# Optimization experiments

Hardware: AMD Instinct MI355X
Metric: run time of the kernel (lower is better)

The kernel has to match this reference:

```python
import jax, jax.numpy as jnp
import numpy as np

EPS_LN = 1e-6
EPS_NORM = 1e-12
MAX_SCALE_MUL = float(np.log(100.0))
H = 16  # num_heads


def _ln(x):
    # affine-free LayerNorm over last dim (torch uses biased variance)
    mu = jnp.mean(x, axis=-1, keepdims=True)
    var = jnp.mean((x - mu) ** 2, axis=-1, keepdims=True)
    return (x - mu) / jnp.sqrt(var + EPS_LN)


def _l2norm(x):
    n = jnp.sqrt(jnp.sum(x * x, axis=-1, keepdims=True))
    return x / jnp.maximum(n, EPS_NORM)


def setup_inputs() -> dict:
    key = jax.random.key(0)
    ks = jax.random.split(key, 12)
    B, L, C = 4, 1024, 1024
    Ccond, Dff = 1024, 4096
    s = lambda fan: 1.0 / np.sqrt(fan)
    return {
        "x": jax.random.normal(ks[0], (B, L, C), jnp.float32),
        "cond": jax.random.normal(ks[1], (B, Ccond), jnp.float32),
        "mat_qkv_w": jax.random.normal(ks[2], (3 * C, C), jnp.float32) * s(C),
        "q_bias": jnp.zeros((C,), jnp.float32),
        "v_bias": jnp.zeros((C,), jnp.float32),
        "scale_mul": jnp.full((1, H, 1, 1), np.log(4.0), jnp.float32),
        "proj_w": jax.random.normal(ks[3], (C, C), jnp.float32) * s(C),
        "proj_b": jnp.zeros((C,), jnp.float32),
        "ada_w": jax.random.normal(ks[4], (6 * C, Ccond), jnp.float32) * s(Ccond),
        "ada_b": jnp.zeros((6 * C,), jnp.float32),
        "fc1_w": jax.random.normal(ks[5], (Dff, C), jnp.float32) * s(C),
        "fc1_b": jnp.zeros((Dff,), jnp.float32),
        "fc2_w": jax.random.normal(ks[6], (C, Dff), jnp.float32) * s(Dff),
        "fc2_b": jnp.zeros((C,), jnp.float32),
    }


def reference(x, cond, mat_qkv_w, q_bias, v_bias, scale_mul, proj_w, proj_b,
              ada_w, ada_b, fc1_w, fc1_b, fc2_w, fc2_b):
    B, L, C = x.shape
    hd = C // H

    # AdaLN modulation params: SiLU -> Linear -> [B,1,6,C]
    ada = jax.nn.silu(cond) @ ada_w.T + ada_b
    ada = ada.reshape(B, 1, 6, C)
    gamma1, gamma2, scale1, scale2, shift1, shift2 = [ada[:, :, i] for i in range(6)]

    # --- attention branch ---
    x1 = _ln(x) * (scale1 + 1.0) + shift1
    qkv_bias = jnp.concatenate([q_bias, jnp.zeros_like(q_bias), v_bias])
    qkv = (x1 @ mat_qkv_w.T + qkv_bias).reshape(B, L, 3, H, hd)
    q, k, v = [jnp.transpose(qkv[:, :, i], (0, 2, 1, 3)) for i in range(3)]  # [B,H,L,hd]

    sm = jnp.exp(jnp.minimum(scale_mul, MAX_SCALE_MUL))  # [1,H,1,1]
    q = _l2norm(q) * sm
    k = _l2norm(k)

    scores = jnp.einsum('bhqd,bhkd->bhqk', q, k)  # scale = 1.0 under l2 norm
    probs = jax.nn.softmax(scores, axis=-1)
    o = jnp.einsum('bhqk,bhkd->bhqd', probs, v)
    o = jnp.transpose(o, (0, 2, 1, 3)).reshape(B, L, C)
    attn_out = o @ proj_w.T + proj_b
    x = x + attn_out * gamma1

    # --- FFN branch ---
    x2 = _ln(x) * (scale2 + 1.0) + shift2
    h = jax.nn.gelu(x2 @ fc1_w.T + fc1_b, approximate=False)
    ffn_out = h @ fc2_w.T + fc2_b
    x = x + ffn_out * gamma2
    return x
```

## Files before the change

### kernel.cpp

```cpp
#include <hip/hip_runtime.h>

typedef __bf16 bf16x8_t __attribute__((ext_vector_type(8)));
typedef bf16x8_t bf16x8 __attribute__((may_alias));
typedef float f32x4 __attribute__((ext_vector_type(4)));
typedef unsigned short u16x4 __attribute__((ext_vector_type(4)));
typedef unsigned short u16x8 __attribute__((ext_vector_type(8)));

#define DEV __device__ __forceinline__

DEV float b2f(unsigned short u) {
  union { unsigned int i; float f; } x; x.i = ((unsigned int)u) << 16; return x.f;
}
DEV unsigned short f2b(float f) {
  union { float f; unsigned int i; } x; x.f = f;
  return (unsigned short)((x.i + 0x7fffu + ((x.i >> 16) & 1u)) >> 16);
}

#define AS1(p) ((__attribute__((address_space(1))) void*)(p))
#define AS3(p) ((__attribute__((address_space(3))) void*)(p))

__global__ __launch_bounds__(256) void k_ada(const float* __restrict__ cond,
                                             const float* __restrict__ w,
                                             const float* __restrict__ bias,
                                             float* __restrict__ out) {
  __shared__ float sc[4096];
  int tt = threadIdx.x;
#pragma unroll
  for (int i = 0; i < 16; ++i) {
    float v = cond[tt + i * 256];
    sc[tt + i * 256] = v / (1.f + __expf(-v));
  }
  __syncthreads();
  int j = blockIdx.x * 4 + (tt >> 6);
  int lane = tt & 63;
  const float* wr = w + (size_t)j * 1024;
  float s0 = 0.f, s1 = 0.f, s2 = 0.f, s3 = 0.f;
#pragma unroll
  for (int u = 0; u < 4; ++u) {
    int k = u * 256 + lane * 4;
    float4 a = *(const float4*)(wr + k);
    float4 c0 = *(const float4*)(sc + k);
    float4 c1 = *(const float4*)(sc + 1024 + k);
    float4 c2 = *(const float4*)(sc + 2048 + k);
    float4 c3 = *(const float4*)(sc + 3072 + k);
    s0 += a.x * c0.x + a.y * c0.y + a.z * c0.z + a.w * c0.w;
    s1 += a.x * c1.x + a.y * c1.y + a.z * c1.z + a.w * c1.w;
    s2 += a.x * c2.x + a.y * c2.y + a.z * c2.z + a.w * c2.w;
    s3 += a.x * c3.x + a.y * c3.y + a.z * c3.z + a.w * c3.w;
  }
#pragma unroll
  for (int o = 1; o < 64; o <<= 1) {
    s0 += __shfl_xor(s0, o); s1 += __shfl_xor(s1, o);
    s2 += __shfl_xor(s2, o); s3 += __shfl_xor(s3, o);
  }
  if (lane == 0) {
    float bb = bias[j];
    out[j] = s0 + bb;
    out[6144 + j] = s1 + bb;
    out[12288 + j] = s2 + bb;
    out[18432 + j] = s3 + bb;
  }
}

__global__ __launch_bounds__(256) void k_castall(const float* __restrict__ q,
                                                 const float* __restrict__ p,
                                                 const float* __restrict__ f1,
                                                 const float* __restrict__ f2,
                                                 unsigned short* __restrict__ wq,
                                                 unsigned short* __restrict__ wp,
                                                 unsigned short* __restrict__ wf1,
                                                 unsigned short* __restrict__ wf2) {
  int i = blockIdx.x * 256 + threadIdx.x;
  for (int v = i; v < 3145728; v += 524288) {
    const float* s; unsigned short* d; int off;
    if (v < 786432) { s = q; d = wq; off = v; }
    else if (v < 1048576) { s = p; d = wp; off = v - 786432; }
    else if (v < 2097152) { s = f1; d = wf1; off = v - 1048576; }
    else { s = f2; d = wf2; off = v - 2097152; }
    float4 x = ((const float4*)s)[off];
    u16x4 o;
    o[0] = f2b(x.x); o[1] = f2b(x.y); o[2] = f2b(x.z); o[3] = f2b(x.w);
    *(u16x4*)(d + (size_t)off * 4) = o;
  }
}

__global__ __launch_bounds__(256) void k_ln_mod(const float* __restrict__ src,
                                                const float* __restrict__ ada,
                                                unsigned short* __restrict__ dst,
                                                int sidx, int hidx) {
  int row = blockIdx.x;
  int b = row >> 10;
  int t = threadIdx.x, lane = t & 63, wv = t >> 6;
  float4 v = *(const float4*)(src + (size_t)row * 1024 + t * 4);
  float s = v.x + v.y + v.z + v.w;
  float s2 = v.x * v.x + v.y * v.y + v.z * v.z + v.w * v.w;
#pragma unroll
  for (int o = 1; o < 64; o <<= 1) { s += __shfl_xor(s, o); s2 += __shfl_xor(s2, o); }
  __shared__ float red[8];
  if (lane == 0) { red[wv] = s; red[4 + wv] = s2; }
  __syncthreads();
  float ts = red[0] + red[1] + red[2] + red[3];
  float ts2 = red[4] + red[5] + red[6] + red[7];
  float mu = ts * (1.f / 1024.f);
  float var = ts2 * (1.f / 1024.f) - mu * mu;
  float rstd = rsqrtf(var + 1e-6f);
  const float* ar = ada + (size_t)b * 6144;
  float4 sc = *(const float4*)(ar + sidx * 1024 + t * 4);
  float4 sh = *(const float4*)(ar + hidx * 1024 + t * 4);
  u16x4 o;
  o[0] = f2b((v.x - mu) * rstd * (sc.x + 1.f) + sh.x);
  o[1] = f2b((v.y - mu) * rstd * (sc.y + 1.f) + sh.y);
  o[2] = f2b((v.z - mu) * rstd * (sc.z + 1.f) + sh.z);
  o[3] = f2b((v.w - mu) * rstd * (sc.w + 1.f) + sh.w);
  *(u16x4*)(dst + (size_t)row * 1024 + t * 4) = o;
}

template <int EPI, int SPLIT>
__global__ __launch_bounds__(512, 4) void k_gemm256(const unsigned short* __restrict__ A,
                                                    const unsigned short* __restrict__ W,
                                                    int N, int lda, int ldb, int nt,
                                                    const float* __restrict__ bias,
                                                    const float* __restrict__ qb,
                                                    const float* __restrict__ vb,
                                                    unsigned short* __restrict__ o0,
                                                    unsigned short* __restrict__ o1,
                                                    unsigned short* __restrict__ o2,
                                                    unsigned short* __restrict__ o3) {
  __shared__ unsigned short LDS[36864];
  const int tid = threadIdx.x;
  const int wv = tid >> 6, lane = tid & 63;
  const int fr = lane & 15, fg = lane >> 4;
  const int wm = wv >> 1, wn = wv & 1;

  const int cpx = gridDim.x >> 3;
  int wid = ((int)blockIdx.x & 7) * cpx + ((int)blockIdx.x >> 3);
  int sp = 0;
  if (SPLIT > 1) { sp = wid & (SPLIT - 1); wid >>= 2; }
  const int nx = N >> 7;
  const int m0 = (wid / nx) * 256, n0 = (wid % nx) * 128;
  const int kbase = sp * (nt << 5);
  unsigned short* outp = (SPLIT > 1) ? (sp == 0 ? o0 : sp == 1 ? o1 : sp == 2 ? o2 : o3) : o0;

  const int sRow = tid >> 2;
  const int sCh = (tid & 3) ^ ((tid >> 3) & 3);
  const unsigned short* aG = A + (size_t)(m0 + sRow) * lda + kbase + sCh * 8;
  const unsigned short* bG = W + (size_t)(n0 + sRow) * ldb + kbase + sCh * 8;

#define STQ3(qi_)                                                                            \
  {                                                                                          \
    unsigned short* d_ = LDS + ((qi_) % 3) * 12288 + tid * 8;                                \
    const int ko_ = (qi_) * 32;                                                              \
    __builtin_amdgcn_global_load_lds(AS1(aG + ko_), AS3(d_), 16, 0, 0);                      \
    __builtin_amdgcn_global_load_lds(AS1(aG + (size_t)128 * lda + ko_), AS3(d_ + 4096), 16, 0, 0); \
    __builtin_amdgcn_global_load_lds(AS1(bG + ko_), AS3(d_ + 8192), 16, 0, 0);               \
  }

  const int rswz = (fr >> 1) & 3;
  const int xc = (fg ^ rswz) << 3;
  const int aOff = (wm * 64 + fr) * 32 + xc;
  const int bOff = 8192 + (wn * 64 + fr) * 32 + xc;

  f32x4 zz = {0.f, 0.f, 0.f, 0.f};
  f32x4 acc[4][4];
#pragma unroll
  for (int i = 0; i < 4; ++i)
#pragma unroll
    for (int j = 0; j < 4; ++j) acc[i][j] = zz;

  STQ3(0); STQ3(1); STQ3(2);
  asm volatile("s_waitcnt vmcnt(6)" ::: "memory");
  __builtin_amdgcn_s_barrier();

#define LDSV(off) (*(const bf16x8*)(LDS + (off)))

  for (int t = 0; t < nt; ++t) {
    if (t >= 1 && t + 2 < nt) STQ3(t + 2);
    const int REG = (t % 3) * 12288;
    bf16x8 b0 = LDSV(REG + bOff);
    bf16x8 b1 = LDSV(REG + bOff + 512);
    bf16x8 b2 = LDSV(REG + bOff + 1024);
    bf16x8 b3 = LDSV(REG + bOff + 1536);
    __builtin_amdgcn_s_setprio(1);
#pragma unroll
    for (int mi = 0; mi < 4; ++mi) {
      bf16x8 a = LDSV(REG + aOff + mi * 512);
      acc[mi][0] = __builtin_amdgcn_mfma_f32_16x16x32_bf16(a, b0, acc[mi][0], 0, 0, 0);
      acc[mi][1] = __builtin_amdgcn_mfma_f32_16x16x32_bf16(a, b1, acc[mi][1], 0, 0, 0);
      acc[mi][2] = __builtin_amdgcn_mfma_f32_16x16x32_bf16(a, b2, acc[mi][2], 0, 0, 0);
      acc[mi][3] = __builtin_amdgcn_mfma_f32_16x16x32_bf16(a, b3, acc[mi][3], 0, 0, 0);
    }
    __builtin_amdgcn_s_setprio(0);
    if (t < nt - 1) {
      if (t + 2 < nt) {
        asm volatile("s_waitcnt vmcnt(3)" ::: "memory");
      } else {
        asm volatile("s_waitcnt vmcnt(0)" ::: "memory");
      }
      __builtin_amdgcn_s_barrier();
    }
  }

  if constexpr (EPI == 0) {
    const int nb = n0 + wn * 64;
    if (nb < 2048) {
      const bool isq = nb < 1024;
      const int h = (nb & 1023) >> 6;
      const float sm = isq ? __expf(fminf(bias[h], 4.6051701859880914f)) : 1.f;
      unsigned short* obase = isq ? o0 : o1;
#pragma unroll
      for (int mi = 0; mi < 4; ++mi) {
#pragma unroll
        for (int r = 0; r < 4; ++r) {
          float v0 = acc[mi][0][r], v1 = acc[mi][1][r], v2 = acc[mi][2][r], v3 = acc[mi][3][r];
          if (isq) {
            v0 += qb[nb + fr]; v1 += qb[nb + 16 + fr];
            v2 += qb[nb + 32 + fr]; v3 += qb[nb + 48 + fr];
          }
          float ss = v0 * v0 + v1 * v1 + v2 * v2 + v3 * v3;
          ss += __shfl_xor(ss, 1); ss += __shfl_xor(ss, 2);
          ss += __shfl_xor(ss, 4); ss += __shfl_xor(ss, 8);
          float scl = sm / fmaxf(sqrtf(ss), 1e-12f);
          int m = m0 + wm * 64 + mi * 16 + fg * 4 + r;
          int b = m >> 10, l = m & 1023;
          unsigned short* dst = obase + ((size_t)(b * 16 + h) * 1024 + l) * 64 + fr;
          dst[0]  = f2b(v0 * scl);
          dst[16] = f2b(v1 * scl);
          dst[32] = f2b(v2 * scl);
          dst[48] = f2b(v3 * scl);
        }
      }
    } else {
#pragma unroll
      for (int mi = 0; mi < 4; ++mi)
#pragma unroll
        for (int ni = 0; ni < 4; ++ni)
#pragma unroll
          for (int r = 0; r < 4; ++r) {
            int m = m0 + wm * 64 + mi * 16 + fg * 4 + r;
            int n = nb + ni * 16 + fr - 2048;
            o2[(size_t)m * 1024 + n] = f2b(acc[mi][ni][r] + vb[n]);
          }
    }
  } else {
#pragma unroll
    for (int mi = 0; mi < 4; ++mi) {
#pragma unroll
      for (int ni = 0; ni < 4; ++ni) {
#pragma unroll
        for (int r = 0; r < 4; ++r) {
          int m = m0 + wm * 64 + mi * 16 + fg * 4 + r;
          int n = n0 + wn * 64 + ni * 16 + fr;
          float v = acc[mi][ni][r];
          if constexpr (EPI == 2) {
            float z = v + bias[n];
            float u = z * (0.7978845608f + 0.0356774081f * z * z);
            float e = __expf(2.f * u);
            float th = 1.f - 2.f / (e + 1.f);
            outp[(size_t)m * N + n] = f2b(0.5f * z * (1.f + th));
          } else {
            outp[(size_t)m * N + n] = f2b(v);
          }
        }
      }
    }
  }
#undef STQ3
#undef LDSV
}

__global__ __launch_bounds__(256) void k_fc2red(const unsigned short* __restrict__ P0,
                                                const unsigned short* __restrict__ P1,
                                                const unsigned short* __restrict__ P2,
                                                const unsigned short* __restrict__ P3,
                                                const float* __restrict__ xmid,
                                                const float* __restrict__ bias,
                                                const float* __restrict__ ada,
                                                float* __restrict__ out) {
  size_t idx = ((size_t)blockIdx.x * 256 + threadIdx.x) * 8;
  int n = (int)(idx & 1023);
  int b = (int)(idx >> 20);
  u16x8 v0 = *(const u16x8*)(P0 + idx);
  u16x8 v1 = *(const u16x8*)(P1 + idx);
  u16x8 v2 = *(const u16x8*)(P2 + idx);
  u16x8 v3 = *(const u16x8*)(P3 + idx);
  const float* gp = ada + (size_t)b * 6144 + 1024 + n;
  const float* bp = bias + n;
  const float* xp = xmid + idx;
  float* op = out + idx;
#pragma unroll
  for (int i = 0; i < 8; ++i) {
    float sum = b2f(v0[i]) + b2f(v1[i]) + b2f(v2[i]) + b2f(v3[i]);
    op[i] = xp[i] + (sum + bp[i]) * gp[i];
  }
}

__global__ __launch_bounds__(512) void k_gemm8(const unsigned short* __restrict__ A,
                                               const unsigned short* __restrict__ W,
                                               int M, int N, int K, int Khalf,
                                               const float* __restrict__ bias,
                                               const float* __restrict__ resid,
                                               const float* __restrict__ ada,
                                               float* __restrict__ outp) {
  __shared__ unsigned short SM[49152];
  const int t = threadIdx.x, lane = t & 63, wv = t >> 6;
  const int grp = wv >> 2, w4 = wv & 3;
  const int wr = w4 >> 1, wc = w4 & 1;
  const int cpx = gridDim.x >> 3;
  const int orig = blockIdx.x;
  const int wid = (orig & 7) * cpx + (orig >> 3);
  const int nx = N >> 7;
  const int m0 = (wid / nx) * 128, n0 = (wid % nx) * 128;

  f32x4 zz = {0.f, 0.f, 0.f, 0.f};
  f32x4 acc[4][4];
#pragma unroll
  for (int i = 0; i < 4; ++i)
#pragma unroll
    for (int j = 0; j < 4; ++j) acc[i][j] = zz;

  const int srow = lane >> 2, scol = (lane & 3) * 8;
  const int kbase = grp * Khalf;
  const unsigned short* aSrc0 = A + (size_t)(m0 + w4 * 16 + srow) * K + kbase + scol;
  const unsigned short* aSrc1 = aSrc0 + (size_t)64 * K;
  const unsigned short* bSrc0 = W + (size_t)(n0 + w4 * 16 + srow) * K + kbase + scol;
  const unsigned short* bSrc1 = bSrc0 + (size_t)64 * K;
  unsigned short* grpA = SM + grp * 24576;

  const int fr = lane & 15, fk = (lane >> 4) * 8;

#define STG8(buf_, k0_)                                                                            \
  {                                                                                                \
    __builtin_amdgcn_global_load_lds(AS1(aSrc0 + (k0_)), AS3(grpA + (buf_)*8192 + w4 * 512), 16, 0, 0); \
    __builtin_amdgcn_global_load_lds(AS1(aSrc1 + (k0_)), AS3(grpA + (buf_)*8192 + 2048 + w4 * 512), 16, 0, 0); \
    __builtin_amdgcn_global_load_lds(AS1(bSrc0 + (k0_)), AS3(grpA + (buf_)*8192 + 4096 + w4 * 512), 16, 0, 0); \
    __builtin_amdgcn_global_load_lds(AS1(bSrc1 + (k0_)), AS3(grpA + (buf_)*8192 + 6144 + w4 * 512), 16, 0, 0); \
  }

  const int nsteps = Khalf >> 5;
  STG8(0, 0);
  STG8(1, 32);
  asm volatile("s_waitcnt vmcnt(4)" ::: "memory");
  __builtin_amdgcn_s_barrier();

  for (int i = 0; i < nsteps; ++i) {
    const int buf = i % 3;
    if (i + 2 < nsteps) STG8((i + 2) % 3, (i + 2) * 32);
    const unsigned short* aRd = grpA + buf * 8192 + (wr * 64 + fr) * 32 + fk;
    const unsigned short* bRd = grpA + buf * 8192 + 4096 + (wc * 64 + fr) * 32 + fk;
    bf16x8 af[4], bfv[4];
#pragma unroll
    for (int q = 0; q < 4; ++q) af[q] = *(const bf16x8*)(aRd + q * 512);
#pragma unroll
    for (int q = 0; q < 4; ++q) bfv[q] = *(const bf16x8*)(bRd + q * 512);
    __builtin_amdgcn_s_setprio(1);
#pragma unroll
    for (int mi = 0; mi < 4; ++mi)
#pragma unroll
      for (int ni = 0; ni < 4; ++ni)
        acc[mi][ni] = __builtin_amdgcn_mfma_f32_16x16x32_bf16(af[mi], bfv[ni], acc[mi][ni], 0, 0, 0);
    __builtin_amdgcn_s_setprio(0);
    if (i < nsteps - 1) {
      if (i + 2 < nsteps) {
        asm volatile("s_waitcnt vmcnt(4)" ::: "memory");
      } else {
        asm volatile("s_waitcnt vmcnt(0)" ::: "memory");
      }
      __builtin_amdgcn_s_barrier();
    }
  }
  __syncthreads();

  float* xch = (float*)SM;
#pragma unroll
  for (int c = 0; c < 16; ++c) {
    if (grp == 1)
      *(f32x4*)&xch[c * 1024 + (w4 * 64 + lane) * 4] = acc[c >> 2][c & 3];
  }
  __syncthreads();
  if (grp == 1) return;
#pragma unroll
  for (int c = 0; c < 16; ++c) {
    f32x4 p = *(const f32x4*)&xch[c * 1024 + (w4 * 64 + lane) * 4];
    acc[c >> 2][c & 3] += p;
  }

  const int fg = lane >> 4;
#pragma unroll
  for (int mi = 0; mi < 4; ++mi) {
#pragma unroll
    for (int ni = 0; ni < 4; ++ni) {
#pragma unroll
      for (int r = 0; r < 4; ++r) {
        int m = m0 + wr * 64 + mi * 16 + fg * 4 + r;
        int n = n0 + wc * 64 + ni * 16 + fr;
        float v = acc[mi][ni][r];
        float g = ada[(size_t)(m >> 10) * 6144 + n];
        outp[(size_t)m * N + n] = resid[(size_t)m * N + n] + (v + bias[n]) * g;
      }
    }
  }
#undef STG8
}

__global__ __launch_bounds__(256) void k_vtrans(const unsigned short* __restrict__ V,
                                                unsigned short* __restrict__ Vt) {
  int bh = blockIdx.y, b = bh >> 4, h = bh & 15;
  int l0 = blockIdx.x * 64;
  __shared__ unsigned short tile[64][72];
  int t = threadIdx.x;
  int lr = t >> 2, dp = (t & 3) * 16;
  const unsigned short* src = V + (size_t)(b * 1024 + l0 + lr) * 1024 + h * 64 + dp;
  *(u16x8*)&tile[lr][dp] = *(const u16x8*)src;
  *(u16x8*)&tile[lr][dp + 8] = *(const u16x8*)(src + 8);
  __syncthreads();
  int d = t >> 2, lp = (t & 3) * 16;
  unsigned short ov[16];
#pragma unroll
  for (int j = 0; j < 16; ++j) {
    int p = lp + j;
    int l = ((p >> 5) * 2 + ((p >> 2) & 1)) * 16 + ((p >> 3) & 3) * 4 + (p & 3);
    ov[j] = tile[l][d];
  }
  unsigned short* dst = Vt + ((size_t)bh * 64 + d) * 1024 + l0 + lp;
  *(u16x8*)dst = *(u16x8*)&ov[0];
  *(u16x8*)(dst + 8) = *(u16x8*)&ov[8];
}

__global__ __launch_bounds__(256) void k_attn(const unsigned short* __restrict__ Qn,
                                              const unsigned short* __restrict__ Kn,
                                              const unsigned short* __restrict__ Vt,
                                              const float* __restrict__ smul,
                                              unsigned short* __restrict__ O) {
  const int qt = blockIdx.x, bh = blockIdx.y;
  const int b = bh >> 4, h = bh & 15;
  const int t = threadIdx.x, lane = t & 63, wv = t >> 6;
  const int fr = lane & 15, fg = lane >> 4;
  __shared__ unsigned short Kb[2][4096];
  __shared__ unsigned short Vb[2][4096];

  const int q0 = qt * 128 + wv * 32;
  const unsigned short* qp = Qn + ((size_t)bh * 1024 + q0 + fr) * 64 + fg * 8;
  bf16x8 qf00 = *(const bf16x8*)qp;
  bf16x8 qf01 = *(const bf16x8*)(qp + 32);
  bf16x8 qf10 = *(const bf16x8*)(qp + 1024);
  bf16x8 qf11 = *(const bf16x8*)(qp + 1024 + 32);

  const float M = __expf(fminf(smul[h], 4.6051701859880914f));

  const int srow = lane >> 3, sc = lane & 7;
  const int xr = (sc ^ srow) * 8;
  const unsigned short* kp0 = Kn + (size_t)bh * 65536 + (size_t)(wv * 16 + srow) * 64 + xr;
  const unsigned short* kp1 = kp0 + 8 * 64;
  const unsigned short* vp0 = Vt + (size_t)bh * 65536 + (size_t)(wv * 16 + srow) * 1024 + xr;
  const unsigned short* vp1 = vp0 + 8 * 1024;

  f32x4 zz = {0.f, 0.f, 0.f, 0.f};
  f32x4 oa0[4], oa1[4];
#pragma unroll
  for (int i = 0; i < 4; ++i) { oa0[i] = zz; oa1[i] = zz; }
  float ls0 = 0.f, ls1 = 0.f;

  {
    unsigned short* kd = &Kb[0][wv * 1024];
    unsigned short* vd = &Vb[0][wv * 1024];
    __builtin_amdgcn_global_load_lds(AS1(kp0), AS3(kd), 16, 0, 0);
    __builtin_amdgcn_global_load_lds(AS1(kp1), AS3(kd + 512), 16, 0, 0);
    __builtin_amdgcn_global_load_lds(AS1(vp0), AS3(vd), 16, 0, 0);
    __builtin_amdgcn_global_load_lds(AS1(vp1), AS3(vd + 512), 16, 0, 0);
  }
  __syncthreads();

  int cur = 0;
  for (int kv = 0; kv < 1024; kv += 64) {
    const int nxt = cur ^ 1;
    if (kv + 64 < 1024) {
      const int ko = (kv + 64) * 64;
      const int vo = kv + 64;
      unsigned short* kd = &Kb[nxt][wv * 1024];
      unsigned short* vd = &Vb[nxt][wv * 1024];
      __builtin_amdgcn_global_load_lds(AS1(kp0 + ko), AS3(kd), 16, 0, 0);
      __builtin_amdgcn_global_load_lds(AS1(kp1 + ko), AS3(kd + 512), 16, 0, 0);
      __builtin_amdgcn_global_load_lds(AS1(vp0 + vo), AS3(vd), 16, 0, 0);
      __builtin_amdgcn_global_load_lds(AS1(vp1 + vo), AS3(vd + 512), 16, 0, 0);
    }

    f32x4 s0[4], s1[4];
    __builtin_amdgcn_s_setprio(1);
#pragma unroll
    for (int ct = 0; ct < 4; ++ct) {
      const int row = ct * 16 + fr, r7 = row & 7;
      const unsigned short* kr = &Kb[cur][row * 64];
      bf16x8 kf0 = *(const bf16x8*)(kr + ((fg ^ r7) << 3));
      bf16x8 kf1 = *(const bf16x8*)(kr + (((4 + fg) ^ r7) << 3));
      f32x4 z0 = __builtin_amdgcn_mfma_f32_16x16x32_bf16(kf0, qf00, zz, 0, 0, 0);
      s0[ct] = __builtin_amdgcn_mfma_f32_16x16x32_bf16(kf1, qf01, z0, 0, 0, 0);
      f32x4 z1 = __builtin_amdgcn_mfma_f32_16x16x32_bf16(kf0, qf10, zz, 0, 0, 0);
      s1[ct] = __builtin_amdgcn_mfma_f32_16x16x32_bf16(kf1, qf11, z1, 0, 0, 0);
    }
    __builtin_amdgcn_s_setprio(0);

    bf16x8 pa0[2], pa1[2];
#pragma unroll
    for (int kg = 0; kg < 2; ++kg) {
      bf16x8 a0, a1;
#pragma unroll
      for (int c2 = 0; c2 < 2; ++c2) {
#pragma unroll
        for (int r = 0; r < 4; ++r) {
          float e0 = __expf(s0[kg * 2 + c2][r] - M);
          float e1 = __expf(s1[kg * 2 + c2][r] - M);
          ls0 += e0; ls1 += e1;
          a0[c2 * 4 + r] = (__bf16)e0;
          a1[c2 * 4 + r] = (__bf16)e1;
        }
      }
      pa0[kg] = a0; pa1[kg] = a1;
    }

    __builtin_amdgcn_s_setprio(1);
#pragma unroll
    for (int kg = 0; kg < 2; ++kg) {
#pragma unroll
      for (int dt = 0; dt < 4; ++dt) {
        const int row = dt * 16 + fr, r7 = row & 7;
        bf16x8 vf = *(const bf16x8*)(&Vb[cur][row * 64] + ((((kg << 2) + fg) ^ r7) << 3));
        oa0[dt] = __builtin_amdgcn_mfma_f32_16x16x32_bf16(pa0[kg], vf, oa0[dt], 0, 0, 0);
        oa1[dt] = __builtin_amdgcn_mfma_f32_16x16x32_bf16(pa1[kg], vf, oa1[dt], 0, 0, 0);
      }
    }
    __builtin_amdgcn_s_setprio(0);
    __syncthreads();
    cur = nxt;
  }

  ls0 += __shfl_xor(ls0, 16); ls0 += __shfl_xor(ls0, 32);
  ls1 += __shfl_xor(ls1, 16); ls1 += __shfl_xor(ls1, 32);

#pragma unroll
  for (int r = 0; r < 4; ++r) {
    float i0 = 1.f / __shfl(ls0, fg * 4 + r);
    float i1 = 1.f / __shfl(ls1, fg * 4 + r);
    unsigned short* ob = O + ((size_t)(b * 1024 + q0 + fg * 4 + r)) * 1024 + h * 64 + fr;
#pragma unroll
    for (int dt = 0; dt < 4; ++dt) {
      ob[dt * 16] = f2b(oa0[dt][r] * i0);
      ob[(size_t)16 * 1024 + dt * 16] = f2b(oa1[dt][r] * i1);
    }
  }
}

extern "C" void kernel_launch(void* const* d_in, const int* in_sizes, int n_in,
                              void* d_out, int out_size, void* d_ws, size_t ws_size,
                              hipStream_t stream) {
  const float* x        = (const float*)d_in[0];
  const float* cond     = (const float*)d_in[1];
  const float* qkv_w    = (const float*)d_in[2];
  const float* q_bias   = (const float*)d_in[3];
  const float* v_bias   = (const float*)d_in[4];
  const float* scale_mul= (const float*)d_in[5];
  const float* proj_w   = (const float*)d_in[6];
  const float* proj_b   = (const float*)d_in[7];
  const float* ada_w    = (const float*)d_in[8];
  const float* ada_b    = (const float*)d_in[9];
  const float* fc1_w    = (const float*)d_in[10];
  const float* fc1_b    = (const float*)d_in[11];
  const float* fc2_w    = (const float*)d_in[12];
  const float* fc2_b    = (const float*)d_in[13];
  float* out = (float*)d_out;
  char* ws = (char*)d_ws;

  unsigned short* WQ   = (unsigned short*)(ws + 0);
  unsigned short* WP   = (unsigned short*)(ws + 6291456);
  unsigned short* WF1  = (unsigned short*)(ws + 8388608);
  unsigned short* WF2  = (unsigned short*)(ws + 16777216);
  float*          ADA  = (float*)(ws + 25182208);
  unsigned short* X1   = (unsigned short*)(ws + 25280512);
  unsigned short* VB   = (unsigned short*)(ws + 33669120);
  float*          XMID = (float*)(ws + 42057728);
  unsigned short* QN   = (unsigned short*)(ws + 58834944);
  unsigned short* KN   = (unsigned short*)(ws + 67223552);
  unsigned short* VT   = (unsigned short*)(ws + 75612160);
  unsigned short* OB   = (unsigned short*)(ws + 84000768);
  unsigned short* HB   = (unsigned short*)(ws + 58834944);
  unsigned short* FP0  = (unsigned short*)(ws + 0);
  unsigned short* FP1  = (unsigned short*)(ws + 8388608);
  unsigned short* FP2  = (unsigned short*)(ws + 25280512);
  unsigned short* FP3  = (unsigned short*)(ws + 33669120);

  (void)in_sizes; (void)n_in; (void)out_size; (void)ws_size;

  k_ada<<<1536, 256, 0, stream>>>(cond, ada_w, ada_b, ADA);
  k_castall<<<2048, 256, 0, stream>>>(qkv_w, proj_w, fc1_w, fc2_w, WQ, WP, WF1, WF2);

  k_ln_mod<<<4096, 256, 0, stream>>>(x, ADA, X1, 2, 4);
  k_gemm256<0, 1><<<384, 512, 0, stream>>>(X1, WQ, 3072, 1024, 1024, 32,
                                           scale_mul, q_bias, v_bias, QN, KN, VB, nullptr);
  k_vtrans<<<dim3(16, 64), 256, 0, stream>>>(VB, VT);
  k_attn<<<dim3(8, 64), 256, 0, stream>>>(QN, KN, VT, scale_mul, OB);
  k_gemm8<<<256, 512, 0, stream>>>(OB, WP, 4096, 1024, 1024, 512,
                                   proj_b, x, ADA, XMID);
  k_ln_mod<<<4096, 256, 0, stream>>>(XMID, ADA, X1, 3, 5);
  k_gemm256<2, 1><<<512, 512, 0, stream>>>(X1, WF1, 4096, 1024, 1024, 32,
                                           fc1_b, nullptr, nullptr, HB, nullptr, nullptr, nullptr);
  k_gemm256<4, 4><<<512, 512, 0, stream>>>(HB, WF2, 1024, 4096, 4096, 32,
                                           nullptr, nullptr, nullptr, FP0, FP1, FP2, FP3);
  k_fc2red<<<2048, 256, 0, stream>>>(FP0, FP1, FP2, FP3, XMID, fc2_b, ADA, out);
}
```

Before: 212.8 us.

## Load GEMM B fragments directly from global into double-buffered registers

The 256x128 GEMM kernel stops staging the weight (B) tile through LDS. Each wave now loads its own B MFMA fragments straight from global memory into two register buffers, alternating them across a loop unrolled by two. Only the A tile still goes through the triple-buffered LDS ring, so LDS use drops and fewer LDS reads feed the MFMAs. In exchange, the four waves that share a column slice each fetch the same B data redundantly with strided 16-byte loads. The vmcnt waits are retuned to the new mix of loads and assume an even tile count.

Measured after the change: 358.2 us. 68.4% more time.

```diff
diff --git a/kernel.cpp b/kernel.cpp
--- a/kernel.cpp
+++ b/kernel.cpp
@@ -126,7 +126,7 @@
                                                     unsigned short* __restrict__ o1,
                                                     unsigned short* __restrict__ o2,
                                                     unsigned short* __restrict__ o3) {
-  __shared__ unsigned short LDS[36864];
+  __shared__ unsigned short LDS[24576];
   const int tid = threadIdx.x;
   const int wv = tid >> 6, lane = tid & 63;
   const int fr = lane & 15, fg = lane >> 4;
@@ -144,21 +144,27 @@
   const int sRow = tid >> 2;
   const int sCh = (tid & 3) ^ ((tid >> 3) & 3);
   const unsigned short* aG = A + (size_t)(m0 + sRow) * lda + kbase + sCh * 8;
-  const unsigned short* bG = W + (size_t)(n0 + sRow) * ldb + kbase + sCh * 8;
-
-#define STQ3(qi_)                                                                            \
+  const unsigned short* bR = W + (size_t)(n0 + wn * 64 + fr) * ldb + kbase + fg * 8;
+
+#define STQ2(qi_)                                                                            \
   {                                                                                          \
-    unsigned short* d_ = LDS + ((qi_) % 3) * 12288 + tid * 8;                                \
+    unsigned short* d_ = LDS + ((qi_) % 3) * 8192 + tid * 8;                                 \
     const int ko_ = (qi_) * 32;                                                              \
     __builtin_amdgcn_global_load_lds(AS1(aG + ko_), AS3(d_), 16, 0, 0);                      \
     __builtin_amdgcn_global_load_lds(AS1(aG + (size_t)128 * lda + ko_), AS3(d_ + 4096), 16, 0, 0); \
-    __builtin_amdgcn_global_load_lds(AS1(bG + ko_), AS3(d_ + 8192), 16, 0, 0);               \
+  }
+
+#define LOADB(D_, T_)                                                                        \
+  {                                                                                          \
+    const unsigned short* bp_ = bR + (size_t)(T_) * 32;                                      \
+    D_[0] = *(const bf16x8*)(bp_);                                                           \
+    D_[1] = *(const bf16x8*)(bp_ + 16 * ldb);                                                \
+    D_[2] = *(const bf16x8*)(bp_ + 32 * ldb);                                                \
+    D_[3] = *(const bf16x8*)(bp_ + 48 * ldb);                                                \
   }
 
   const int rswz = (fr >> 1) & 3;
-  const int xc = (fg ^ rswz) << 3;
-  const int aOff = (wm * 64 + fr) * 32 + xc;
-  const int bOff = 8192 + (wn * 64 + fr) * 32 + xc;
+  const int aOff = (wm * 64 + fr) * 32 + ((fg ^ rswz) << 3);
 
   f32x4 zz = {0.f, 0.f, 0.f, 0.f};
   f32x4 acc[4][4];
@@ -167,37 +173,43 @@
 #pragma unroll
     for (int j = 0; j < 4; ++j) acc[i][j] = zz;
 
-  STQ3(0); STQ3(1); STQ3(2);
-  asm volatile("s_waitcnt vmcnt(6)" ::: "memory");
+  bf16x8 bc[4], bn[4];
+
+  STQ2(0); STQ2(1); STQ2(2);
+  LOADB(bc, 0); LOADB(bn, 1);
+  asm volatile("s_waitcnt vmcnt(0)" ::: "memory");
   __builtin_amdgcn_s_barrier();
 
 #define LDSV(off) (*(const bf16x8*)(LDS + (off)))
 
-  for (int t = 0; t < nt; ++t) {
-    if (t >= 1 && t + 2 < nt) STQ3(t + 2);
-    const int REG = (t % 3) * 12288;
-    bf16x8 b0 = LDSV(REG + bOff);
-    bf16x8 b1 = LDSV(REG + bOff + 512);
-    bf16x8 b2 = LDSV(REG + bOff + 1024);
-    bf16x8 b3 = LDSV(REG + bOff + 1536);
-    __builtin_amdgcn_s_setprio(1);
-#pragma unroll
-    for (int mi = 0; mi < 4; ++mi) {
-      bf16x8 a = LDSV(REG + aOff + mi * 512);
-      acc[mi][0] = __builtin_amdgcn_mfma_f32_16x16x32_bf16(a, b0, acc[mi][0], 0, 0, 0);
-      acc[mi][1] = __builtin_amdgcn_mfma_f32_16x16x32_bf16(a, b1, acc[mi][1], 0, 0, 0);
-      acc[mi][2] = __builtin_amdgcn_mfma_f32_16x16x32_bf16(a, b2, acc[mi][2], 0, 0, 0);
-      acc[mi][3] = __builtin_amdgcn_mfma_f32_16x16x32_bf16(a, b3, acc[mi][3], 0, 0, 0);
-    }
-    __builtin_amdgcn_s_setprio(0);
-    if (t < nt - 1) {
-      if (t + 2 < nt) {
-        asm volatile("s_waitcnt vmcnt(3)" ::: "memory");
-      } else {
-        asm volatile("s_waitcnt vmcnt(0)" ::: "memory");
-      }
-      __builtin_amdgcn_s_barrier();
-    }
+#define STEP(T_, BC_, BN_)                                                                   \
+  {                                                                                          \
+    if ((T_) >= 1 && (T_) + 1 < nt) LOADB(BN_, (T_) + 1);                                    \
+    __builtin_amdgcn_sched_barrier(0);                                                       \
+    if ((T_) >= 1 && (T_) + 2 < nt) STQ2((T_) + 2);                                          \
+    const int REG_ = ((T_) % 3) * 8192;                                                      \
+    __builtin_amdgcn_s_setprio(1);                                                           \
+    _Pragma("unroll")                                                                        \
+    for (int mi_ = 0; mi_ < 4; ++mi_) {                                                      \
+      bf16x8 a_ = LDSV(REG_ + aOff + mi_ * 512);                                             \
+      acc[mi_][0] = __builtin_amdgcn_mfma_f32_16x16x32_bf16(a_, BC_[0], acc[mi_][0], 0, 0, 0); \
+      acc[mi_][1] = __builtin_amdgcn_mfma_f32_16x16x32_bf16(a_, BC_[1], acc[mi_][1], 0, 0, 0); \
+      acc[mi_][2] = __builtin_amdgcn_mfma_f32_16x16x32_bf16(a_, BC_[2], acc[mi_][2], 0, 0, 0); \
+      acc[mi_][3] = __builtin_amdgcn_mfma_f32_16x16x32_bf16(a_, BC_[3], acc[mi_][3], 0, 0, 0); \
+    }                                                                                        \
+    __builtin_amdgcn_s_setprio(0);                                                           \
+    if ((T_) + 2 < nt) {                                                                     \
+      asm volatile("s_waitcnt vmcnt(2)" ::: "memory");                                       \
+      __builtin_amdgcn_s_barrier();                                                          \
+    } else if ((T_) < nt - 1) {                                                              \
+      asm volatile("s_waitcnt vmcnt(0)" ::: "memory");                                       \
+      __builtin_amdgcn_s_barrier();                                                          \
+    }                                                                                        \
+  }
+
+  for (int t = 0; t < nt; t += 2) {
+    STEP(t, bc, bn)
+    STEP(t + 1, bn, bc)
   }
 
   if constexpr (EPI == 0) {
@@ -264,8 +276,10 @@
       }
     }
   }
-#undef STQ3
+#undef STQ2
+#undef LOADB
 #undef LDSV
+#undef STEP
 }
 
 __global__ __launch_bounds__(256) void k_fc2red(const unsigned short* __restrict__ P0,
```
